# Performance work log

Measured on AMD Instinct MI355X. Metric: run time of the kernel, lower is better.

The kernel has to match this reference:

```python
import jax, jax.numpy as jnp
import numpy as np

H = 16        # num_attention_heads
KV = 4        # num_key_value_heads
HD = 128      # head_dim = hidden // H
N_REP = H // KV
ROPE_THETA = 10000.0


def _rope_cos_sin(T, dtype):
    inv_freq = 1.0 / (ROPE_THETA ** (jnp.arange(0, HD, 2, dtype=jnp.float32) / HD))
    pos = jnp.arange(T, dtype=jnp.float32)
    freqs = pos[:, None] * inv_freq[None, :]            # [T, HD/2]
    emb = jnp.concatenate([freqs, freqs], axis=-1)      # [T, HD]
    return jnp.cos(emb).astype(dtype), jnp.sin(emb).astype(dtype)


def _rotate_half(t):
    t1, t2 = jnp.split(t, 2, axis=-1)
    return jnp.concatenate([-t2, t1], axis=-1)


def setup_inputs() -> dict:
    key = jax.random.key(0)
    k1, k2, k3 = jax.random.split(key, 3)
    B, T, C = 2, 2048, 2048
    x = jax.random.normal(k1, (B, T, C), dtype=jnp.float32)
    attention_mask = jnp.ones((B, T), dtype=jnp.float32)
    w_qkv = jax.random.normal(k2, ((H + 2 * KV) * HD, C), dtype=jnp.float32) * 0.02
    w_proj = jax.random.normal(k3, (C, C), dtype=jnp.float32) * 0.02
    return {"x": x, "attention_mask": attention_mask, "w_qkv": w_qkv, "w_proj": w_proj}


def reference(x, attention_mask, w_qkv, w_proj):
    B, T, C = x.shape
    dtype = x.dtype
    neg = jnp.finfo(dtype).min

    # additive mask: causal (-big above diagonal) + padding ((1-mask)*min)
    i = jnp.arange(T)
    causal = jnp.where(i[None, :] <= i[:, None], 0.0, neg).astype(dtype)  # [T,T]
    add_mask = (1.0 - attention_mask)[:, None, None, :] * neg + causal[None, None]  # [B,1,T,T]

    # fused QKV projection
    qkv = jnp.einsum('btc,oc->bto', x, w_qkv)
    q = qkv[..., : H * HD].reshape(B, T, H, HD)
    k = qkv[..., H * HD : (H + KV) * HD].reshape(B, T, KV, HD)
    v = qkv[..., (H + KV) * HD :].reshape(B, T, KV, HD)

    # RoPE on q and k
    cos, sin = _rope_cos_sin(T, dtype)
    cos = cos[None, :, None, :]
    sin = sin[None, :, None, :]
    q = q * cos + _rotate_half(q) * sin
    k = k * cos + _rotate_half(k) * sin

    # GQA: repeat_interleave KV heads
    k = jnp.repeat(k, N_REP, axis=2)  # [B,T,H,HD]
    v = jnp.repeat(v, N_REP, axis=2)

    # [B,H,T,HD]
    q, k, v = (jnp.transpose(t, (0, 2, 1, 3)) for t in (q, k, v))

    scores = jnp.einsum('bhqd,bhkd->bhqk', q, k) * (1.0 / np.sqrt(HD))
    att = jax.nn.softmax(scores + add_mask, axis=-1)
    y = jnp.einsum('bhqk,bhkd->bhqd', att, v)
    y = jnp.transpose(y, (0, 2, 1, 3)).reshape(B, T, C)
    return jnp.einsum('btc,oc->bto', y, w_proj)
```

## Files before the change

### kernel.cpp

```cpp
#include <hip/hip_runtime.h>
#include <hip/hip_bf16.h>
#include <stdint.h>

typedef unsigned short u16;
typedef __attribute__((ext_vector_type(4))) float f32x4;
typedef __attribute__((ext_vector_type(16))) float f32x16;
typedef __attribute__((ext_vector_type(8))) __bf16 bf16x8;

#define NB 2
#define NT 2048
#define NC 2048
#define NH 16
#define NKV 4
#define HD 128
#define NQKV 3072
#define SCALE2 0.12751739f

__device__ __forceinline__ u16 f2bf(float f) {
  union { float f; uint32_t u; } c; c.f = f;
  uint32_t u = c.u + 0x7fffu + ((c.u >> 16) & 1u);
  return (u16)(u >> 16);
}
__device__ __forceinline__ float bf2f(u16 h) {
  union { uint32_t u; float f; } c; c.u = ((uint32_t)h) << 16;
  return c.f;
}
__device__ __forceinline__ uint32_t packbf2(float a, float b) {
  return (uint32_t)f2bf(a) | ((uint32_t)f2bf(b) << 16);
}

__device__ __forceinline__ void gload16(const void* g, void* lds) {
  __builtin_amdgcn_global_load_lds(
      (__attribute__((address_space(1))) void*)(uintptr_t)g,
      (__attribute__((address_space(3))) void*)(uint32_t)(uintptr_t)lds,
      16, 0, 0);
}

__global__ void cvt_bf16_kernel(const float* __restrict__ in, u16* __restrict__ out, int n4) {
  int i = blockIdx.x * blockDim.x + threadIdx.x;
  if (i >= n4) return;
  float4 v = ((const float4*)in)[i];
  uint32_t lo = (uint32_t)f2bf(v.x) | ((uint32_t)f2bf(v.y) << 16);
  uint32_t hi = (uint32_t)f2bf(v.z) | ((uint32_t)f2bf(v.w) << 16);
  ((uint2*)out)[i] = make_uint2(lo, hi);
}

__global__ void rope_tab_kernel(float* __restrict__ tab) {
  int idx = blockIdx.x * blockDim.x + threadIdx.x;
  int t = idx >> 6, i = idx & 63;
  float inv = expf(-(float)(2 * i) * (9.210340371976184f / 128.f));
  float f = (float)t * inv;
  tab[t * 128 + i] = cosf(f);
  tab[t * 128 + 64 + i] = sinf(f);
}

__global__ void rope_apply_kernel(const u16* __restrict__ qkv, const float* __restrict__ tab,
                                  u16* __restrict__ Q, u16* __restrict__ K) {
  int idx = blockIdx.x * blockDim.x + threadIdx.x;
  int i = idx & 63;
  int rest = idx >> 6;
  int hh = rest % 20;
  int bt = rest / 20;
  int t = bt & (NT - 1);
  int b = bt >> 11;
  const u16* src_row = qkv + (long)bt * NQKV;
  float c = tab[t * 128 + i], s = tab[t * 128 + 64 + i];
  if (hh < NH) {
    const u16* sp = src_row + hh * HD;
    float x0 = bf2f(sp[i]), x1 = bf2f(sp[i + 64]);
    u16* dp = Q + ((long)(b * NH + hh) * NT + t) * HD;
    dp[i] = f2bf((x0 * c - x1 * s) * SCALE2);
    dp[i + 64] = f2bf((x1 * c + x0 * s) * SCALE2);
  } else {
    int kh = hh - NH;
    const u16* sp = src_row + (NH + kh) * HD;
    float x0 = bf2f(sp[i]), x1 = bf2f(sp[i + 64]);
    u16* dp = K + ((long)(b * NKV + kh) * NT + t) * HD;
    dp[i] = f2bf(x0 * c - x1 * s);
    dp[i + 64] = f2bf(x1 * c + x0 * s);
  }
}

__global__ void vtrans_kernel(const u16* __restrict__ qkv, u16* __restrict__ Vt) {
  __shared__ u16 tile[64][72];
  const int t0 = (blockIdx.x >> 1) * 64;
  const int d0 = (blockIdx.x & 1) * 64;
  const int bkh = blockIdx.y;
  const int tid = threadIdx.x;
  const int tr = tid >> 2;
  const int tc = (tid & 3) * 16;
  const u16* src = qkv + ((long)((bkh >> 2) * NT) + t0 + tr) * NQKV +
                   (NH + NKV) * HD + (bkh & 3) * HD + d0 + tc;
  uint4 v0 = *(const uint4*)(src);
  uint4 v1 = *(const uint4*)(src + 8);
  *(uint4*)&tile[tr][tc] = v0;
  *(uint4*)&tile[tr][tc + 8] = v1;
  __syncthreads();
  const int dr = tid >> 2;
  const int tcc = (tid & 3) * 16;
  uint32_t pk[8];
#pragma unroll
  for (int e = 0; e < 8; ++e) {
    u16 a = tile[tcc + 2 * e][dr];
    u16 bq = tile[tcc + 2 * e + 1][dr];
    pk[e] = (uint32_t)a | ((uint32_t)bq << 16);
  }
  uint32_t tmp;
  tmp = pk[2]; pk[2] = pk[4]; pk[4] = tmp;
  tmp = pk[3]; pk[3] = pk[5]; pk[5] = tmp;
  const int d = d0 + dr;
  const int t = t0 + tcc;
  u16* dst = Vt + (long)bkh * HD * NT + (long)(d >> 1) * (2 * NT) +
             (t >> 6) * 128 + (d & 1) * 64 + (t & 48);
  *(uint4*)(dst) = *(uint4*)&pk[0];
  *(uint4*)(dst + 8) = *(uint4*)&pk[4];
}

template <int OUT_BF16>
__global__ __launch_bounds__(256) void gemm_bt_kernel(const u16* __restrict__ A,
                                                      const u16* __restrict__ Bm,
                                                      void* __restrict__ Cm,
                                                      int M, int N, int K) {
  __shared__ __align__(16) u16 As[128 * 32];
  __shared__ __align__(16) u16 Bs[128 * 32];
  const int tid = threadIdx.x;
  const int lane = tid & 63;
  const int wid = tid >> 6;
  const long row0 = (long)blockIdx.y * 128;
  const long col0 = (long)blockIdx.x * 128;
  const int wr = (wid >> 1) * 64;
  const int wc = (wid & 1) * 64;
  const int g = lane >> 4;
  const int r = lane & 15;
  const int crow = lane >> 2;
  const int ccol = (lane & 3) * 8;
  const int c0 = wid * 2, c1 = wid * 2 + 1;

  f32x4 acc[4][4] = {};

  const u16* Abase0 = A + (row0 + c0 * 16 + crow) * (long)K + ccol;
  const u16* Abase1 = A + (row0 + c1 * 16 + crow) * (long)K + ccol;
  const u16* Bbase0 = Bm + (col0 + c0 * 16 + crow) * (long)K + ccol;
  const u16* Bbase1 = Bm + (col0 + c1 * 16 + crow) * (long)K + ccol;

  for (int k0 = 0; k0 < K; k0 += 32) {
    gload16(Abase0 + k0, &As[c0 * 512]);
    gload16(Abase1 + k0, &As[c1 * 512]);
    gload16(Bbase0 + k0, &Bs[c0 * 512]);
    gload16(Bbase1 + k0, &Bs[c1 * 512]);
    __syncthreads();
    bf16x8 af[4], bfr[4];
#pragma unroll
    for (int mi = 0; mi < 4; ++mi)
      af[mi] = *(const bf16x8*)&As[(wr + mi * 16 + r) * 32 + 8 * g];
#pragma unroll
    for (int ni = 0; ni < 4; ++ni)
      bfr[ni] = *(const bf16x8*)&Bs[(wc + ni * 16 + r) * 32 + 8 * g];
#pragma unroll
    for (int mi = 0; mi < 4; ++mi)
#pragma unroll
      for (int ni = 0; ni < 4; ++ni)
        acc[mi][ni] = __builtin_amdgcn_mfma_f32_16x16x32_bf16(af[mi], bfr[ni], acc[mi][ni], 0, 0, 0);
    __syncthreads();
  }
#pragma unroll
  for (int mi = 0; mi < 4; ++mi)
#pragma unroll
    for (int ni = 0; ni < 4; ++ni)
#pragma unroll
      for (int j = 0; j < 4; ++j) {
        long rr = row0 + wr + mi * 16 + g * 4 + j;
        long cc = col0 + wc + ni * 16 + r;
        float v = acc[mi][ni][j];
        if (OUT_BF16) ((u16*)Cm)[rr * N + cc] = f2bf(v);
        else          ((float*)Cm)[rr * N + cc] = v;
      }
}

__global__ __launch_bounds__(256, 2) void attn_kernel(const u16* __restrict__ Qg,
                                                      const u16* __restrict__ Kg,
                                                      const u16* __restrict__ Vtg,
                                                      const float* __restrict__ amask,
                                                      u16* __restrict__ Y) {
  __shared__ __align__(16) u16 Ks[2][64 * 128];
  __shared__ __align__(16) u16 Vs[2][64 * 128];
  const int tid = threadIdx.x, lane = tid & 63, wid = tid >> 6;
  const int ql = lane & 31, hi = lane >> 5;
  const int id = blockIdx.x;
  const int h = id & 15;
  const int xp = (id >> 4) & 7;
  const int b = (id >> 7) & 1;
  const int half = id >> 8;
  const int qt = half ? 15 - xp : xp;
  const int q0 = qt * 128;
  const int kh = h >> 2;

  const u16* Kbh = Kg + (long)(b * NKV + kh) * NT * HD;
  const u16* Vtbh = Vtg + (long)(b * NKV + kh) * HD * NT;
  const u16* Qbh = Qg + (long)(b * NH + h) * NT * HD;
  const float* am_b = amask + b * NT;

  const int total = 2 * qt + 2;

  const int srow = lane >> 4;
  const int schunk = lane & 15;
  auto stageK = [&](u16* dst, int kv0) {
#pragma unroll
    for (int ii = 0; ii < 4; ++ii) {
      int kvl = wid * 16 + ii * 4 + srow;
      const u16* src = Kbh + (long)(kv0 + kvl) * HD + ((schunk ^ (kvl & 15)) * 8);
      gload16(src, dst + (wid * 16 + ii * 4) * 128);
    }
  };
  auto stageV = [&](u16* dst, int kv0) {
    const u16* vb = Vtbh + (kv0 >> 6) * 128;
#pragma unroll
    for (int ii = 0; ii < 4; ++ii) {
      int R = wid * 16 + ii * 4 + srow;
      const u16* src = vb + (long)R * (2 * NT) + ((schunk ^ (R & 15)) * 8);
      gload16(src, dst + (wid * 16 + ii * 4) * 128);
    }
  };

  stageK(Ks[0], 0);
  stageV(Vs[0], 0);
  bf16x8 qf[8];
  {
    const u16* Qrow = Qbh + (long)(q0 + wid * 32 + ql) * HD;
#pragma unroll
    for (int ks = 0; ks < 8; ++ks)
      qf[ks] = *(const bf16x8*)(Qrow + ks * 16 + 8 * hi);
  }

  float m = -INFINITY;
  f32x4 lacc = {};
  f32x16 o[4] = {};
  int buf = 0;
  const int qi = q0 + wid * 32 + ql;

  for (int i = 0; i < total; ++i) {
    const int kv0 = i * 64;

    float4 am0[4], am1[4];
#pragma unroll
    for (int u = 0; u < 4; ++u) {
      am0[u] = *(const float4*)(am_b + kv0 + 8 * u + 4 * hi);
      am1[u] = *(const float4*)(am_b + kv0 + 32 + 8 * u + 4 * hi);
    }
    __builtin_amdgcn_sched_barrier(0);

    if (i + 1 < total) {
      stageK(Ks[buf ^ 1], (i + 1) * 64);
      stageV(Vs[buf ^ 1], (i + 1) * 64);
      __builtin_amdgcn_sched_barrier(0);
      asm volatile("s_waitcnt vmcnt(16)" ::: "memory");
    } else {
      __builtin_amdgcn_sched_barrier(0);
      asm volatile("s_waitcnt vmcnt(8)" ::: "memory");
    }
    __builtin_amdgcn_sched_barrier(0);
    __builtin_amdgcn_s_barrier();
    __builtin_amdgcn_sched_barrier(0);

    const char* Ksb = (const char*)Ks[buf];
    const char* Vsb = (const char*)Vs[buf];

    f32x16 s0 = {}, s1 = {};
    __builtin_amdgcn_s_setprio(1);
#pragma unroll
    for (int ks = 0; ks < 8; ++ks) {
      bf16x8 kf0 = *(const bf16x8*)(Ksb + ql * 256 + (((2 * ks + hi) ^ (ql & 15)) * 16));
      bf16x8 kf1 = *(const bf16x8*)(Ksb + (32 + ql) * 256 + (((2 * ks + hi) ^ (ql & 15)) * 16));
      s0 = __builtin_amdgcn_mfma_f32_32x32x16_bf16(kf0, qf[ks], s0, 0, 0, 0);
      s1 = __builtin_amdgcn_mfma_f32_32x32x16_bf16(kf1, qf[ks], s1, 0, 0, 0);
    }
    __builtin_amdgcn_s_setprio(0);

    if (i >= 2 * qt) {
#pragma unroll
      for (int reg = 0; reg < 16; ++reg) {
        int kvl = (reg & 3) + 8 * (reg >> 2) + 4 * hi;
        if (kv0 + kvl > qi) s0[reg] = -INFINITY;
        if (kv0 + 32 + kvl > qi) s1[reg] = -INFINITY;
      }
    }

    float mxl = s0[0];
#pragma unroll
    for (int reg = 0; reg < 16; ++reg) { mxl = fmaxf(mxl, s0[reg]); mxl = fmaxf(mxl, s1[reg]); }
    if (!__all(mxl <= m + 8.f)) {
      float mx = fmaxf(mxl, __shfl_xor(mxl, 32));
      float mnew = fmaxf(m, mx);
      float alpha = exp2f(m - mnew);
      m = mnew;
      lacc *= alpha;
#pragma unroll
      for (int dblk = 0; dblk < 4; ++dblk) o[dblk] *= alpha;
    }

#pragma unroll
    for (int reg = 0; reg < 16; ++reg) {
      float p0 = exp2f(s0[reg] - m) * (&am0[reg >> 2].x)[reg & 3];
      float p1 = exp2f(s1[reg] - m) * (&am1[reg >> 2].x)[reg & 3];
      s0[reg] = p0; s1[reg] = p1;
      lacc[reg & 3] += p0 + p1;
    }

    bf16x8 pb[4];
#pragma unroll
    for (int ks = 0; ks < 4; ++ks) {
      union { __bf16 hh[8]; bf16x8 v; } pk;
      const int base = 8 * (ks & 1);
#pragma unroll
      for (int j = 0; j < 8; ++j)
        pk.hh[j] = (__bf16)((ks >= 2) ? s1[base + j] : s0[base + j]);
      pb[ks] = pk.v;
    }

    __builtin_amdgcn_s_setprio(1);
#pragma unroll
    for (int ks = 0; ks < 4; ++ks) {
#pragma unroll
      for (int dblk = 0; dblk < 4; ++dblk) {
        int drow = dblk * 16 + (ql >> 1);
        int gr = ((ql & 1) * 8 + 2 * ks + hi) ^ (drow & 15);
        bf16x8 va = *(const bf16x8*)(Vsb + drow * 256 + gr * 16);
        o[dblk] = __builtin_amdgcn_mfma_f32_32x32x16_bf16(va, pb[ks], o[dblk], 0, 0, 0);
      }
    }
    __builtin_amdgcn_s_setprio(0);

    __builtin_amdgcn_sched_barrier(0);
    __builtin_amdgcn_s_barrier();
    __builtin_amdgcn_sched_barrier(0);
    buf ^= 1;
  }

  {
    float l = (lacc[0] + lacc[1]) + (lacc[2] + lacc[3]);
    l += __shfl_xor(l, 32);
    float invl = 1.f / l;
    u16* Yrow = Y + ((long)b * NT + qi) * NC + h * HD;
#pragma unroll
    for (int dblk = 0; dblk < 4; ++dblk)
#pragma unroll
      for (int u = 0; u < 4; ++u) {
        int d = dblk * 32 + 8 * u + 4 * hi;
        int r0 = 4 * u;
        *(uint2*)(Yrow + d) = make_uint2(
            packbf2(o[dblk][r0] * invl, o[dblk][r0 + 1] * invl),
            packbf2(o[dblk][r0 + 2] * invl, o[dblk][r0 + 3] * invl));
      }
  }
}

extern "C" void kernel_launch(void* const* d_in, const int* in_sizes, int n_in,
                              void* d_out, int out_size, void* d_ws, size_t ws_size,
                              hipStream_t stream) {
  const float* x = (const float*)d_in[0];
  const float* amask = (const float*)d_in[1];
  const float* w_qkv = (const float*)d_in[2];
  const float* w_proj = (const float*)d_in[3];

  const long MT = (long)NB * NT;
  char* ws = (char*)d_ws;
  size_t off = 0;
  auto carve = [&](size_t bytes) -> char* {
    char* p = ws + off;
    off += (bytes + 255) & ~(size_t)255;
    return p;
  };
  u16* xb   = (u16*)carve((size_t)MT * NC * 2);
  u16* wqb  = (u16*)carve((size_t)NQKV * NC * 2);
  u16* wpb  = (u16*)carve((size_t)NC * NC * 2);
  u16* qkvb = (u16*)carve((size_t)MT * NQKV * 2);
  float* tab = (float*)carve((size_t)NT * 128 * 4);

  u16* Qb = xb;
  u16* Kb = wqb;
  u16* Vtb = wqb + (size_t)NB * NKV * NT * HD;
  u16* Yb = qkvb;

  {
    int n4 = (int)(MT * NC / 4);
    cvt_bf16_kernel<<<dim3((n4 + 255) / 256), dim3(256), 0, stream>>>(x, xb, n4);
    n4 = (int)((long)NQKV * NC / 4);
    cvt_bf16_kernel<<<dim3((n4 + 255) / 256), dim3(256), 0, stream>>>(w_qkv, wqb, n4);
    n4 = (int)((long)NC * NC / 4);
    cvt_bf16_kernel<<<dim3((n4 + 255) / 256), dim3(256), 0, stream>>>(w_proj, wpb, n4);
  }
  rope_tab_kernel<<<dim3(NT * 64 / 256), dim3(256), 0, stream>>>(tab);
  gemm_bt_kernel<1><<<dim3(NQKV / 128, MT / 128), dim3(256), 0, stream>>>(xb, wqb, qkvb, (int)MT, NQKV, NC);
  rope_apply_kernel<<<dim3(NB * NT * 20 * 64 / 256), dim3(256), 0, stream>>>(qkvb, tab, Qb, Kb);
  vtrans_kernel<<<dim3(NT / 64 * 2, NB * NKV), dim3(256), 0, stream>>>(qkvb, Vtb);
  attn_kernel<<<dim3(512), dim3(256), 0, stream>>>(Qb, Kb, Vtb, amask, Yb);
  gemm_bt_kernel<0><<<dim3(NC / 128, MT / 128), dim3(256), 0, stream>>>(Yb, wpb, d_out, (int)MT, NC, NC);
}
```

Before: 237.4 us.

## Replace GEMM with double-buffered 256x128 swizzled tile kernel; simplify attention sync

The QKV and output projection GEMMs switch from a single-buffered 128x128, K=32 kernel to a 512-thread 256x128 tile. It uses K=64 stages, double-buffered LDS and an XOR swizzle, so global loads for the next stage overlap MFMA work on the current one. The attention loop drops its hand-tuned vmcnt waits and the barrier at the top of the loop in favour of a single __syncthreads at the end, and the padding-mask loads move closer to where they are used. The larger tiles give fewer blocks per launch, which risks uneven wave quantisation on the QKV GEMM. The full-fence __syncthreads may also reduce how much of the attention prefetch overlaps with compute.

```diff
diff --git a/kernel.cpp b/kernel.cpp
--- a/kernel.cpp
+++ b/kernel.cpp
@@ -117,60 +117,93 @@
 }
 
 template <int OUT_BF16>
-__global__ __launch_bounds__(256) void gemm_bt_kernel(const u16* __restrict__ A,
-                                                      const u16* __restrict__ Bm,
-                                                      void* __restrict__ Cm,
-                                                      int M, int N, int K) {
-  __shared__ __align__(16) u16 As[128 * 32];
-  __shared__ __align__(16) u16 Bs[128 * 32];
-  const int tid = threadIdx.x;
-  const int lane = tid & 63;
-  const int wid = tid >> 6;
-  const long row0 = (long)blockIdx.y * 128;
+__global__ __launch_bounds__(512, 1) void gemm256_kernel(const u16* __restrict__ A,
+                                                         const u16* __restrict__ Bm,
+                                                         void* __restrict__ Cm,
+                                                         int M, int N, int K) {
+  __shared__ __align__(16) u16 As[2][256 * 64];
+  __shared__ __align__(16) u16 Bs[2][128 * 64];
+  const int tid = threadIdx.x, lane = tid & 63, wid = tid >> 6;
+  const int wr = wid >> 1, wc = wid & 1;
+  const int g = lane >> 4, r = lane & 15;
+  const long row0 = (long)blockIdx.y * 256;
   const long col0 = (long)blockIdx.x * 128;
-  const int wr = (wid >> 1) * 64;
-  const int wc = (wid & 1) * 64;
-  const int g = lane >> 4;
-  const int r = lane & 15;
-  const int crow = lane >> 2;
-  const int ccol = (lane & 3) * 8;
-  const int c0 = wid * 2, c1 = wid * 2 + 1;
+  const int lrow = lane >> 3;
+  const int lch = lane & 7;
 
   f32x4 acc[4][4] = {};
 
-  const u16* Abase0 = A + (row0 + c0 * 16 + crow) * (long)K + ccol;
-  const u16* Abase1 = A + (row0 + c1 * 16 + crow) * (long)K + ccol;
-  const u16* Bbase0 = Bm + (col0 + c0 * 16 + crow) * (long)K + ccol;
-  const u16* Bbase1 = Bm + (col0 + c1 * 16 + crow) * (long)K + ccol;
-
-  for (int k0 = 0; k0 < K; k0 += 32) {
-    gload16(Abase0 + k0, &As[c0 * 512]);
-    gload16(Abase1 + k0, &As[c1 * 512]);
-    gload16(Bbase0 + k0, &Bs[c0 * 512]);
-    gload16(Bbase1 + k0, &Bs[c1 * 512]);
-    __syncthreads();
-    bf16x8 af[4], bfr[4];
-#pragma unroll
-    for (int mi = 0; mi < 4; ++mi)
-      af[mi] = *(const bf16x8*)&As[(wr + mi * 16 + r) * 32 + 8 * g];
+  auto stage = [&](int bufi, int kt) {
+    const int k0 = kt * 64;
+    u16* Ad = As[bufi];
+    u16* Bd = Bs[bufi];
+#pragma unroll
+    for (int ii = 0; ii < 4; ++ii) {
+      int rowl = wid * 32 + ii * 8 + lrow;
+      const u16* src = A + (row0 + rowl) * (long)K + k0 + ((lch ^ (rowl & 7)) * 8);
+      gload16(src, Ad + (wid * 32 + ii * 8) * 64);
+    }
+#pragma unroll
+    for (int ii = 0; ii < 2; ++ii) {
+      int rowl = wid * 16 + ii * 8 + lrow;
+      const u16* src = Bm + (col0 + rowl) * (long)K + k0 + ((lch ^ (rowl & 7)) * 8);
+      gload16(src, Bd + (wid * 16 + ii * 8) * 64);
+    }
+  };
+
+  const int nt = K / 64;
+  stage(0, 0);
+  int buf = 0;
+  for (int t = 0; t < nt; ++t) {
+    if (t + 1 < nt) {
+      stage(buf ^ 1, t + 1);
+      __builtin_amdgcn_sched_barrier(0);
+      asm volatile("s_waitcnt vmcnt(6)" ::: "memory");
+    } else {
+      __builtin_amdgcn_sched_barrier(0);
+      asm volatile("s_waitcnt vmcnt(0)" ::: "memory");
+    }
+    __builtin_amdgcn_sched_barrier(0);
+    __builtin_amdgcn_s_barrier();
+    __builtin_amdgcn_sched_barrier(0);
+
+    const char* Ab = (const char*)As[buf];
+    const char* Bb = (const char*)Bs[buf];
+#pragma unroll
+    for (int ks = 0; ks < 2; ++ks) {
+      bf16x8 af[4], bfv[4];
+#pragma unroll
+      for (int mi = 0; mi < 4; ++mi) {
+        int row = wr * 64 + mi * 16 + r;
+        af[mi] = *(const bf16x8*)(Ab + row * 128 + (((4 * ks + g) ^ (row & 7)) * 16));
+      }
+#pragma unroll
+      for (int ni = 0; ni < 4; ++ni) {
+        int row = wc * 64 + ni * 16 + r;
+        bfv[ni] = *(const bf16x8*)(Bb + row * 128 + (((4 * ks + g) ^ (row & 7)) * 16));
+      }
+      __builtin_amdgcn_s_setprio(1);
+#pragma unroll
+      for (int mi = 0; mi < 4; ++mi)
+#pragma unroll
+        for (int ni = 0; ni < 4; ++ni)
+          acc[mi][ni] = __builtin_amdgcn_mfma_f32_16x16x32_bf16(af[mi], bfv[ni], acc[mi][ni], 0, 0, 0);
+      __builtin_amdgcn_s_setprio(0);
+    }
+    __builtin_amdgcn_sched_barrier(0);
+    __builtin_amdgcn_s_barrier();
+    __builtin_amdgcn_sched_barrier(0);
+    buf ^= 1;
+  }
+
+#pragma unroll
+  for (int mi = 0; mi < 4; ++mi)
 #pragma unroll
     for (int ni = 0; ni < 4; ++ni)
-      bfr[ni] = *(const bf16x8*)&Bs[(wc + ni * 16 + r) * 32 + 8 * g];
-#pragma unroll
-    for (int mi = 0; mi < 4; ++mi)
-#pragma unroll
-      for (int ni = 0; ni < 4; ++ni)
-        acc[mi][ni] = __builtin_amdgcn_mfma_f32_16x16x32_bf16(af[mi], bfr[ni], acc[mi][ni], 0, 0, 0);
-    __syncthreads();
-  }
-#pragma unroll
-  for (int mi = 0; mi < 4; ++mi)
-#pragma unroll
-    for (int ni = 0; ni < 4; ++ni)
 #pragma unroll
       for (int j = 0; j < 4; ++j) {
-        long rr = row0 + wr + mi * 16 + g * 4 + j;
-        long cc = col0 + wc + ni * 16 + r;
+        long rr = row0 + wr * 64 + mi * 16 + g * 4 + j;
+        long cc = col0 + wc * 64 + ni * 16 + r;
         float v = acc[mi][ni][j];
         if (OUT_BF16) ((u16*)Cm)[rr * N + cc] = f2bf(v);
         else          ((float*)Cm)[rr * N + cc] = v;
@@ -222,8 +255,6 @@
     }
   };
 
-  stageK(Ks[0], 0);
-  stageV(Vs[0], 0);
   bf16x8 qf[8];
   {
     const u16* Qrow = Qbh + (long)(q0 + wid * 32 + ql) * HD;
@@ -231,6 +262,10 @@
     for (int ks = 0; ks < 8; ++ks)
       qf[ks] = *(const bf16x8*)(Qrow + ks * 16 + 8 * hi);
   }
+
+  stageK(Ks[0], 0);
+  stageV(Vs[0], 0);
+  __syncthreads();
 
   float m = -INFINITY;
   f32x4 lacc = {};
@@ -241,26 +276,10 @@
   for (int i = 0; i < total; ++i) {
     const int kv0 = i * 64;
 
-    float4 am0[4], am1[4];
-#pragma unroll
-    for (int u = 0; u < 4; ++u) {
-      am0[u] = *(const float4*)(am_b + kv0 + 8 * u + 4 * hi);
-      am1[u] = *(const float4*)(am_b + kv0 + 32 + 8 * u + 4 * hi);
-    }
-    __builtin_amdgcn_sched_barrier(0);
-
     if (i + 1 < total) {
       stageK(Ks[buf ^ 1], (i + 1) * 64);
       stageV(Vs[buf ^ 1], (i + 1) * 64);
-      __builtin_amdgcn_sched_barrier(0);
-      asm volatile("s_waitcnt vmcnt(16)" ::: "memory");
-    } else {
-      __builtin_amdgcn_sched_barrier(0);
-      asm volatile("s_waitcnt vmcnt(8)" ::: "memory");
-    }
-    __builtin_amdgcn_sched_barrier(0);
-    __builtin_amdgcn_s_barrier();
-    __builtin_amdgcn_sched_barrier(0);
+    }
 
     const char* Ksb = (const char*)Ks[buf];
     const char* Vsb = (const char*)Vs[buf];
@@ -298,6 +317,12 @@
       for (int dblk = 0; dblk < 4; ++dblk) o[dblk] *= alpha;
     }
 
+    float4 am0[4], am1[4];
+#pragma unroll
+    for (int u = 0; u < 4; ++u) {
+      am0[u] = *(const float4*)(am_b + kv0 + 8 * u + 4 * hi);
+      am1[u] = *(const float4*)(am_b + kv0 + 32 + 8 * u + 4 * hi);
+    }
 #pragma unroll
     for (int reg = 0; reg < 16; ++reg) {
       float p0 = exp2f(s0[reg] - m) * (&am0[reg >> 2].x)[reg & 3];
@@ -330,9 +355,7 @@
     }
     __builtin_amdgcn_s_setprio(0);
 
-    __builtin_amdgcn_sched_barrier(0);
-    __builtin_amdgcn_s_barrier();
-    __builtin_amdgcn_sched_barrier(0);
+    __syncthreads();
     buf ^= 1;
   }
 
@@ -390,9 +413,9 @@
     cvt_bf16_kernel<<<dim3((n4 + 255) / 256), dim3(256), 0, stream>>>(w_proj, wpb, n4);
   }
   rope_tab_kernel<<<dim3(NT * 64 / 256), dim3(256), 0, stream>>>(tab);
-  gemm_bt_kernel<1><<<dim3(NQKV / 128, MT / 128), dim3(256), 0, stream>>>(xb, wqb, qkvb, (int)MT, NQKV, NC);
+  gemm256_kernel<1><<<dim3(NQKV / 128, MT / 256), dim3(512), 0, stream>>>(xb, wqb, qkvb, (int)MT, NQKV, NC);
   rope_apply_kernel<<<dim3(NB * NT * 20 * 64 / 256), dim3(256), 0, stream>>>(qkvb, tab, Qb, Kb);
   vtrans_kernel<<<dim3(NT / 64 * 2, NB * NKV), dim3(256), 0, stream>>>(qkvb, Vtb);
   attn_kernel<<<dim3(512), dim3(256), 0, stream>>>(Qb, Kb, Vtb, amask, Yb);
-  gemm_bt_kernel<0><<<dim3(NC / 128, MT / 128), dim3(256), 0, stream>>>(Yb, wpb, d_out, (int)MT, NC, NC);
-}
+  gemm256_kernel<0><<<dim3(NC / 128, MT / 256), dim3(512), 0, stream>>>(Yb, wpb, d_out, (int)MT, NC, NC);
+}
```

Measured after the change: 221.5 us. -6.7%, faster.
